# Kernel optimization log

Hardware: AMD Instinct MI355X
Metric: run time of the kernel (lower is better)

The kernel has to match this reference:

```python
import jax, jax.numpy as jnp
import numpy as np

GROUP = 128  # W4A16 quantization group size along the input (reduction) dim


def dequant(q, s, z):
    """Dequantize int4 weights. q: [out, in] ints in [0,16); s, z: [out, in//GROUP]."""
    out_f, in_f = q.shape
    g = in_f // GROUP
    qf = q.reshape(out_f, g, GROUP).astype(s.dtype)
    w = (qf - z[:, :, None]) * s[:, :, None]
    return w.reshape(out_f, in_f)


def setup_inputs() -> dict:
    key = jax.random.key(0)
    ks = jax.random.split(key, 11)
    H, I = 4096, 11008
    B, S = 4, 2048
    x = jax.random.normal(ks[0], (B, S, H), dtype=jnp.float32)
    qw_gate = jax.random.randint(ks[1], (I, H), 0, 16, dtype=jnp.int32)
    qw_up = jax.random.randint(ks[2], (I, H), 0, 16, dtype=jnp.int32)
    qw_down = jax.random.randint(ks[3], (H, I), 0, 16, dtype=jnp.int32)
    # scales small so dequantized weights have realistic magnitude; zeros in [0,16)
    s_gate = jax.random.uniform(ks[4], (I, H // GROUP), dtype=jnp.float32) * 0.01
    z_gate = jax.random.uniform(ks[5], (I, H // GROUP), dtype=jnp.float32) * 16.0
    s_up = jax.random.uniform(ks[6], (I, H // GROUP), dtype=jnp.float32) * 0.01
    z_up = jax.random.uniform(ks[7], (I, H // GROUP), dtype=jnp.float32) * 16.0
    s_down = jax.random.uniform(ks[8], (H, I // GROUP), dtype=jnp.float32) * 0.01
    z_down = jax.random.uniform(ks[9], (H, I // GROUP), dtype=jnp.float32) * 16.0
    return {
        "x": x,
        "qw_gate": qw_gate, "qw_up": qw_up, "qw_down": qw_down,
        "s_gate": s_gate, "z_gate": z_gate,
        "s_up": s_up, "z_up": z_up,
        "s_down": s_down, "z_down": z_down,
    }


def reference(x, qw_gate, qw_up, qw_down, s_gate, z_gate, s_up, z_up, s_down, z_down):
    # W4A16 SwiGLU MLP: down( silu(gate(x)) * up(x) )
    Wg = dequant(qw_gate, s_gate, z_gate)   # [I, H]
    Wu = dequant(qw_up, s_up, z_up)         # [I, H]
    Wd = dequant(qw_down, s_down, z_down)   # [H, I]
    g = jnp.einsum('bsh,ih->bsi', x, Wg)
    u = jnp.einsum('bsh,ih->bsi', x, Wu)
    h = jax.nn.silu(g) * u
    return jnp.einsum('bsi,hi->bsh', h, Wd)
```

## Files before the change

### kernel.cpp

```cpp
#include <hip/hip_runtime.h>
#include <hip/hip_fp16.h>

typedef __attribute__((ext_vector_type(8))) short s16x8;
typedef __attribute__((ext_vector_type(8))) _Float16 f16x8;
typedef __attribute__((ext_vector_type(4))) float f32x4;

__global__ void cvt_f32_to_f16_kernel(const float* __restrict__ in,
                                      __half* __restrict__ out, long n) {
  long i = (long)blockIdx.x * blockDim.x + threadIdx.x;
  long stride = (long)gridDim.x * blockDim.x;
  const float4* p4 = (const float4*)in;
  for (long j = i; j * 8 < n; j += stride) {
    float4 a = p4[j * 2];
    float4 b = p4[j * 2 + 1];
    union { s16x8 v; __half2 h2[4]; } w;
    w.h2[0] = __floats2half2_rn(a.x, a.y);
    w.h2[1] = __floats2half2_rn(a.z, a.w);
    w.h2[2] = __floats2half2_rn(b.x, b.y);
    w.h2[3] = __floats2half2_rn(b.z, b.w);
    *(s16x8*)(out + j * 8) = w.v;
  }
}

__global__ void pack_kernel(const int* __restrict__ q, uint32_t* __restrict__ p,
                            long n8) {
  long i = (long)blockIdx.x * blockDim.x + threadIdx.x;
  long stride = (long)gridDim.x * blockDim.x;
  for (; i < n8; i += stride) {
    int4 a = ((const int4*)q)[2 * i];
    int4 b = ((const int4*)q)[2 * i + 1];
    uint32_t w = (uint32_t)a.x | ((uint32_t)a.y << 4) | ((uint32_t)a.z << 8) |
                 ((uint32_t)a.w << 12) | ((uint32_t)b.x << 16) |
                 ((uint32_t)b.y << 20) | ((uint32_t)b.z << 24) |
                 ((uint32_t)b.w << 28);
    p[i] = w;
  }
}

__device__ __forceinline__ s16x8 dq_compute(int4 q0, int4 q1, float s, float z) {
  __half hs = __float2half(s);
  __half2 s2 = __halves2half2(hs, hs);
  __half hc = __float2half(-(64.f + z) * s);
  __half2 c2 = __halves2half2(hc, hc);
  uint32_t b0 = 0x54005400u + ((uint32_t)q0.x << 4) + ((uint32_t)q0.y << 20);
  uint32_t b1 = 0x54005400u + ((uint32_t)q0.z << 4) + ((uint32_t)q0.w << 20);
  uint32_t b2 = 0x54005400u + ((uint32_t)q1.x << 4) + ((uint32_t)q1.y << 20);
  uint32_t b3 = 0x54005400u + ((uint32_t)q1.z << 4) + ((uint32_t)q1.w << 20);
  union { s16x8 v; __half2 h2[4]; } w;
  w.h2[0] = __hfma2(*(__half2*)&b0, s2, c2);
  w.h2[1] = __hfma2(*(__half2*)&b1, s2, c2);
  w.h2[2] = __hfma2(*(__half2*)&b2, s2, c2);
  w.h2[3] = __hfma2(*(__half2*)&b3, s2, c2);
  return w.v;
}

__device__ __forceinline__ s16x8 dq8(uint32_t w, __half2 s2, __half2 c2) {
  union { s16x8 v; __half2 h2[4]; } r;
#pragma unroll
  for (int i = 0; i < 4; ++i) {
    uint32_t t = (w >> (8 * i)) & 0xFFu;
    uint32_t b = 0x54005400u + ((t & 15u) << 4) + ((t >> 4) << 20);
    r.h2[i] = __hfma2(*(__half2*)&b, s2, c2);
  }
  return r.v;
}

__device__ __forceinline__ int xcd_swz(int w0, int nwg) {
  const int q = nwg >> 3, r = nwg & 7;
  const int xcd = w0 & 7, idx = w0 >> 3;
  const int base = (xcd < r) ? xcd * (q + 1) : r * (q + 1) + (xcd - r) * q;
  return base + idx;
}

template <int PKG, int PKU>
__global__ __launch_bounds__(512, 2)
void gateup_kernel(const __half* __restrict__ Xh,
                   const int* __restrict__ Qg, const uint32_t* __restrict__ Pg,
                   const int* __restrict__ Qu, const uint32_t* __restrict__ Pu,
                   const float* __restrict__ Sg, const float* __restrict__ Zg,
                   const float* __restrict__ Su, const float* __restrict__ Zu,
                   __half* __restrict__ Pan, int mbs) {
  constexpr int H = 4096, I = 11008, G = 32;
  const int wg = xcd_swz(blockIdx.x, gridDim.x);
  const int mb = wg % mbs;
  const int nb = wg / mbs;
  const int m0 = mb * 256;
  const int n0 = nb * 128;
  const int tid = threadIdx.x;
  const int lane = tid & 63;
  const int wave = tid >> 6;
  const int wm = (wave >> 1) * 64, wn = (wave & 1) * 64;
  const int l15 = lane & 15, lq = lane >> 4;
  const int rsw = (l15 & 7) << 3;

  __shared__ __half As[2][256][64];
  __shared__ __half Bg[2][128][64];
  __shared__ __half Bu[2][128][64];

  f32x4 accg[4][4], accu[4][4];
#pragma unroll
  for (int i = 0; i < 4; ++i)
#pragma unroll
    for (int j = 0; j < 4; ++j) {
      accg[i][j] = {0.f, 0.f, 0.f, 0.f};
      accu[i][j] = {0.f, 0.f, 0.f, 0.f};
    }

  const int arowD = tid >> 3;
  const int acolD = (((tid & 7) ^ ((tid >> 3) & 7)) << 3);
  const int qrow = tid >> 2, qcol0 = (tid & 3) * 16, qsw = (qrow & 7) << 3;
  const int*      qPg = Qg + (size_t)(n0 + qrow) * H + qcol0;
  const int*      qPu = Qu + (size_t)(n0 + qrow) * H + qcol0;
  const uint32_t* pPg = Pg + (size_t)(n0 + qrow) * (H / 8) + (tid & 3) * 2;
  const uint32_t* pPu = Pu + (size_t)(n0 + qrow) * (H / 8) + (tid & 3) * 2;
  const float* sPg = Sg + (size_t)(n0 + qrow) * G;
  const float* zPg = Zg + (size_t)(n0 + qrow) * G;
  const float* sPu = Su + (size_t)(n0 + qrow) * G;
  const float* zPu = Zu + (size_t)(n0 + qrow) * G;

  int4 qG[4], qU[4];
  uint32_t wG0, wG1, wU0, wU1;
  float sG, zG, sU, zU;

#define STAGE_A(buf, kk)                                              \
  {                                                                   \
    const int _k = (kk);                                              \
    _Pragma("unroll")                                                 \
    for (int c = 0; c < 4; ++c) {                                     \
      const __half* src = Xh + (size_t)(m0 + c * 64 + arowD) * H + _k + acolD; \
      __half* dst = &As[buf][0][0] + (size_t)(c * 512 + tid) * 8;     \
      __builtin_amdgcn_global_load_lds((const __attribute__((address_space(1))) void*)src, \
                                       (__attribute__((address_space(3))) void*)dst, 16, 0, 0); \
    }                                                                 \
  }
#define LOAD_Q(kk)                                                    \
  {                                                                   \
    const int _k = (kk);                                              \
    if (PKG) { wG0 = pPg[_k >> 3]; wG1 = pPg[(_k >> 3) + 1]; }        \
    else {                                                            \
      _Pragma("unroll")                                               \
      for (int i = 0; i < 4; ++i) qG[i] = ((const int4*)(qPg + _k))[i]; \
    }                                                                 \
    if (PKU) { wU0 = pPu[_k >> 3]; wU1 = pPu[(_k >> 3) + 1]; }        \
    else {                                                            \
      _Pragma("unroll")                                               \
      for (int i = 0; i < 4; ++i) qU[i] = ((const int4*)(qPu + _k))[i]; \
    }                                                                 \
    sG = sPg[_k >> 7]; zG = zPg[_k >> 7];                             \
    sU = sPu[_k >> 7]; zU = zPu[_k >> 7];                             \
  }
#define WRITE_B(buf)                                                  \
  {                                                                   \
    if (PKG) {                                                        \
      __half h1 = __float2half(sG);                                   \
      __half2 s2 = __halves2half2(h1, h1);                            \
      __half h2 = __float2half(-(64.f + zG) * sG);                    \
      __half2 c2 = __halves2half2(h2, h2);                            \
      *(s16x8*)&Bg[buf][qrow][(qcol0 + 0) ^ qsw] = dq8(wG0, s2, c2);  \
      *(s16x8*)&Bg[buf][qrow][(qcol0 + 8) ^ qsw] = dq8(wG1, s2, c2);  \
    } else {                                                          \
      *(s16x8*)&Bg[buf][qrow][(qcol0 + 0) ^ qsw] = dq_compute(qG[0], qG[1], sG, zG); \
      *(s16x8*)&Bg[buf][qrow][(qcol0 + 8) ^ qsw] = dq_compute(qG[2], qG[3], sG, zG); \
    }                                                                 \
    if (PKU) {                                                        \
      __half h3 = __float2half(sU);                                   \
      __half2 s3 = __halves2half2(h3, h3);                            \
      __half h4 = __float2half(-(64.f + zU) * sU);                    \
      __half2 c3 = __halves2half2(h4, h4);                            \
      *(s16x8*)&Bu[buf][qrow][(qcol0 + 0) ^ qsw] = dq8(wU0, s3, c3);  \
      *(s16x8*)&Bu[buf][qrow][(qcol0 + 8) ^ qsw] = dq8(wU1, s3, c3);  \
    } else {                                                          \
      *(s16x8*)&Bu[buf][qrow][(qcol0 + 0) ^ qsw] = dq_compute(qU[0], qU[1], sU, zU); \
      *(s16x8*)&Bu[buf][qrow][(qcol0 + 8) ^ qsw] = dq_compute(qU[2], qU[3], sU, zU); \
    }                                                                 \
  }
#define MFMA_BUF(buf)                                                 \
  {                                                                   \
    __builtin_amdgcn_s_setprio(1);                                    \
    _Pragma("unroll")                                                 \
    for (int kk = 0; kk < 2; ++kk) {                                  \
      const int cbase = (kk * 32 + lq * 8) ^ rsw;                     \
      f16x8 af[4];                                                    \
      _Pragma("unroll")                                               \
      for (int i = 0; i < 4; ++i)                                     \
        af[i] = *(const f16x8*)&As[buf][wm + i * 16 + l15][cbase];    \
      _Pragma("unroll")                                               \
      for (int j = 0; j < 4; ++j) {                                   \
        f16x8 bg = *(const f16x8*)&Bg[buf][wn + j * 16 + l15][cbase]; \
        f16x8 bu = *(const f16x8*)&Bu[buf][wn + j * 16 + l15][cbase]; \
        _Pragma("unroll")                                             \
        for (int i = 0; i < 4; ++i) {                                 \
          accg[i][j] = __builtin_amdgcn_mfma_f32_16x16x32_f16(af[i], bg, accg[i][j], 0, 0, 0); \
          accu[i][j] = __builtin_amdgcn_mfma_f32_16x16x32_f16(af[i], bu, accu[i][j], 0, 0, 0); \
        }                                                             \
      }                                                               \
    }                                                                 \
    __builtin_amdgcn_s_setprio(0);                                    \
  }

  const int nt = H / 64;
  STAGE_A(0, 0)
  LOAD_Q(0)
  WRITE_B(0)
  __syncthreads();

  int p = 0;
  for (int t = 0; t < nt; ++t) {
    if (t + 1 < nt) {
      STAGE_A(p ^ 1, (t + 1) * 64)
      LOAD_Q((t + 1) * 64)
    }
    MFMA_BUF(p)
    if (t + 1 < nt) WRITE_B(p ^ 1)
    __syncthreads();
    p ^= 1;
  }
#undef STAGE_A
#undef LOAD_Q
#undef WRITE_B
#undef MFMA_BUF

#pragma unroll
  for (int i = 0; i < 4; ++i)
#pragma unroll
    for (int j = 0; j < 4; ++j)
#pragma unroll
      for (int r = 0; r < 4; ++r) {
        const int row = m0 + wm + i * 16 + lq * 4 + r;
        const int col = n0 + wn + j * 16 + l15;
        float g = accg[i][j][r];
        float u = accu[i][j][r];
        float hv = (g / (1.f + __expf(-g))) * u;
        Pan[(size_t)row * I + col] = __float2half(hv);
      }
}

template <int PK>
__global__ __launch_bounds__(512, 2)
void down_kernel(const __half* __restrict__ Hws,
                 const int* __restrict__ Qd, const uint32_t* __restrict__ QdP,
                 const float* __restrict__ Sd, const float* __restrict__ Zd,
                 float* __restrict__ Out, int mbs) {
  constexpr int K = 11008, N = 4096, G = 86;
  const int wg = xcd_swz(blockIdx.x, gridDim.x);
  const int mb = wg % mbs;
  const int nb = wg / mbs;
  const int m0 = mb * 256, n0 = nb * 128;
  const int tid = threadIdx.x;
  const int lane = tid & 63;
  const int wave = tid >> 6;
  const int wm = (wave >> 1) * 64, wn = (wave & 1) * 64;
  const int l15 = lane & 15, lq = lane >> 4;
  const int rsw = (l15 & 7) << 3;

  __shared__ __half As[2][256][64];
  __shared__ __half Bs[2][128][64];

  f32x4 acc[4][4];
#pragma unroll
  for (int i = 0; i < 4; ++i)
#pragma unroll
    for (int j = 0; j < 4; ++j) acc[i][j] = {0.f, 0.f, 0.f, 0.f};

  const int arowD = tid >> 3;
  const int acolD = (((tid & 7) ^ ((tid >> 3) & 7)) << 3);
  const int qrow = tid >> 2, qcol0 = (tid & 3) * 16, qsw = (qrow & 7) << 3;
  const int*      qP  = Qd  + (size_t)(n0 + qrow) * K + qcol0;
  const uint32_t* qPp = QdP + (size_t)(n0 + qrow) * (K / 8) + (tid & 3) * 2;
  const float* sP = Sd + (size_t)(n0 + qrow) * G;
  const float* zP = Zd + (size_t)(n0 + qrow) * G;

  int4 qA[4], qB[4];
  uint32_t wA0, wA1, wB0, wB1;
  float sA, zA, sB, zB;

#define STAGE_A(buf, kk)                                              \
  {                                                                   \
    const int _k = (kk);                                              \
    _Pragma("unroll")                                                 \
    for (int c = 0; c < 4; ++c) {                                     \
      const __half* src = Hws + (size_t)(m0 + c * 64 + arowD) * K + _k + acolD; \
      __half* dst = &As[buf][0][0] + (size_t)(c * 512 + tid) * 8;     \
      __builtin_amdgcn_global_load_lds((const __attribute__((address_space(1))) void*)src, \
                                       (__attribute__((address_space(3))) void*)dst, 16, 0, 0); \
    }                                                                 \
  }
#define LOAD_Q(set, kk)                                               \
  {                                                                   \
    const int _k = (kk);                                              \
    if (PK) {                                                         \
      w##set##0 = qPp[_k >> 3]; w##set##1 = qPp[(_k >> 3) + 1];       \
    } else {                                                          \
      _Pragma("unroll")                                               \
      for (int i = 0; i < 4; ++i) q##set[i] = ((const int4*)(qP + _k))[i]; \
    }                                                                 \
    s##set = sP[_k >> 7]; z##set = zP[_k >> 7];                       \
  }
#define WRITE_B(buf, set)                                             \
  {                                                                   \
    if (PK) {                                                         \
      __half hs = __float2half(s##set);                               \
      __half2 s2 = __halves2half2(hs, hs);                            \
      __half hc = __float2half(-(64.f + z##set) * s##set);            \
      __half2 c2 = __halves2half2(hc, hc);                            \
      *(s16x8*)&Bs[buf][qrow][(qcol0 + 0) ^ qsw] = dq8(w##set##0, s2, c2); \
      *(s16x8*)&Bs[buf][qrow][(qcol0 + 8) ^ qsw] = dq8(w##set##1, s2, c2); \
    } else {                                                          \
      *(s16x8*)&Bs[buf][qrow][(qcol0 + 0) ^ qsw] = dq_compute(q##set[0], q##set[1], s##set, z##set); \
      *(s16x8*)&Bs[buf][qrow][(qcol0 + 8) ^ qsw] = dq_compute(q##set[2], q##set[3], s##set, z##set); \
    }                                                                 \
  }
#define MFMA_BUF(buf)                                                 \
  {                                                                   \
    __builtin_amdgcn_s_setprio(1);                                    \
    _Pragma("unroll")                                                 \
    for (int kk = 0; kk < 2; ++kk) {                                  \
      const int cbase = (kk * 32 + lq * 8) ^ rsw;                     \
      f16x8 af[4];                                                    \
      _Pragma("unroll")                                               \
      for (int i = 0; i < 4; ++i)                                     \
        af[i] = *(const f16x8*)&As[buf][wm + i * 16 + l15][cbase];    \
      _Pragma("unroll")                                               \
      for (int j = 0; j < 4; ++j) {                                   \
        f16x8 bf = *(const f16x8*)&Bs[buf][wn + j * 16 + l15][cbase]; \
        _Pragma("unroll")                                             \
        for (int i = 0; i < 4; ++i)                                   \
          acc[i][j] = __builtin_amdgcn_mfma_f32_16x16x32_f16(af[i], bf, acc[i][j], 0, 0, 0); \
      }                                                               \
    }                                                                 \
    __builtin_amdgcn_s_setprio(0);                                    \
  }

  const int nt = K / 64;
  STAGE_A(0, 0)
  LOAD_Q(A, 0)
  LOAD_Q(B, 64)
  WRITE_B(0, A)
  __syncthreads();

  for (int t = 0; t < nt; t += 2) {
    if (t + 1 < nt) STAGE_A(1, (t + 1) * 64)
    if (t + 2 < nt) LOAD_Q(A, (t + 2) * 64)
    MFMA_BUF(0)
    if (t + 1 < nt) WRITE_B(1, B)
    __syncthreads();
    if (t + 2 < nt) STAGE_A(0, (t + 2) * 64)
    if (t + 3 < nt) LOAD_Q(B, (t + 3) * 64)
    MFMA_BUF(1)
    if (t + 2 < nt) WRITE_B(0, A)
    __syncthreads();
  }
#undef STAGE_A
#undef LOAD_Q
#undef WRITE_B
#undef MFMA_BUF

#pragma unroll
  for (int i = 0; i < 4; ++i)
#pragma unroll
    for (int j = 0; j < 4; ++j)
#pragma unroll
      for (int r = 0; r < 4; ++r) {
        const int row = m0 + wm + i * 16 + lq * 4 + r;
        const int col = n0 + wn + j * 16 + l15;
        Out[(size_t)row * N + col] = acc[i][j][r];
      }
}

extern "C" void kernel_launch(void* const* d_in, const int* in_sizes, int n_in,
                              void* d_out, int out_size, void* d_ws, size_t ws_size,
                              hipStream_t stream) {
  const float* x  = (const float*)d_in[0];
  const int* qg   = (const int*)d_in[1];
  const int* qu   = (const int*)d_in[2];
  const int* qd   = (const int*)d_in[3];
  const float* sg = (const float*)d_in[4];
  const float* zg = (const float*)d_in[5];
  const float* su = (const float*)d_in[6];
  const float* zu = (const float*)d_in[7];
  const float* sd = (const float*)d_in[8];
  const float* zd = (const float*)d_in[9];
  float* out = (float*)d_out;

  const int M = 8192, H = 4096, I = 11008;
  const long N8 = (long)I * H / 8;

  const int PD_MAX = 1375, PG_MAX = 2751, PU_MAX = 4127;
  uint32_t* Pd = (uint32_t*)d_out;
  uint32_t* Pg = Pd + N8;
  uint32_t* Pu = Pg + N8;

  pack_kernel<<<2048, 256, 0, stream>>>(qd, Pd, N8);
  pack_kernel<<<2048, 256, 0, stream>>>(qg, Pg, N8);
  pack_kernel<<<2048, 256, 0, stream>>>(qu, Pu, N8);

  long mc = (long)(ws_size / ((size_t)I * 2));
  mc &= ~255L;
  if (mc > 2048) mc = 2048;
  if (mc < 256) mc = 256;
  const int Mc = (int)mc;
  __half* wsh = (__half*)d_ws;

  int mb_arr[64], mbs_arr[64];
  int nch = 0;
  for (int mb = 0; mb < M; mb += Mc) {
    mb_arr[nch] = mb;
    mbs_arr[nch] = ((M - mb < Mc) ? (M - mb) : Mc) / 256;
    ++nch;
  }

  int destr = M;
  for (int c = nch - 1; c >= 0; --c) {
    const int mbase = mb_arr[c];
    const int mbs = mbs_arr[c];
    const int rows = mbs * 256;
    const int xrows = rows / 2;
    const int wsxlo = mbase + rows - xrows;
    __half* wsx = (__half*)(out + (size_t)wsxlo * H);

    cvt_f32_to_f16_kernel<<<1024, 256, 0, stream>>>(
        x + (size_t)mbase * H, wsx, (long)rows * H);
    if (wsxlo < destr) destr = wsxlo;

    const bool g_pk = (PG_MAX < destr);
    const bool u_pk = (PU_MAX < destr);
    const bool d_pk = (PD_MAX < destr) && (PD_MAX < mbase);

    if (g_pk && u_pk)
      gateup_kernel<1, 1><<<mbs * (I / 128), 512, 0, stream>>>(
          wsx, qg, Pg, qu, Pu, sg, zg, su, zu, wsh, mbs);
    else if (g_pk)
      gateup_kernel<1, 0><<<mbs * (I / 128), 512, 0, stream>>>(
          wsx, qg, Pg, qu, Pu, sg, zg, su, zu, wsh, mbs);
    else
      gateup_kernel<0, 0><<<mbs * (I / 128), 512, 0, stream>>>(
          wsx, qg, Pg, qu, Pu, sg, zg, su, zu, wsh, mbs);

    if (d_pk)
      down_kernel<1><<<mbs * 32, 512, 0, stream>>>(
          wsh, qd, Pd, sd, zd, out + (size_t)mbase * H, mbs);
    else
      down_kernel<0><<<mbs * 32, 512, 0, stream>>>(
          wsh, qd, Pd, sd, zd, out + (size_t)mbase * H, mbs);

    if (mbase < destr) destr = mbase;
  }
}
```

Before: 3.039 ms.

## Fuse pack/convert prep and fold next chunk's x conversion into GEMM grids

```diff
diff --git a/kernel.cpp b/kernel.cpp
--- a/kernel.cpp
+++ b/kernel.cpp
@@ -5,35 +5,51 @@
 typedef __attribute__((ext_vector_type(8))) _Float16 f16x8;
 typedef __attribute__((ext_vector_type(4))) float f32x4;
 
+__device__ __forceinline__ void cvt_unit(const float4* __restrict__ p4,
+                                         __half* __restrict__ out, long j) {
+  float4 a = p4[j * 2];
+  float4 b = p4[j * 2 + 1];
+  union { s16x8 v; __half2 h2[4]; } w;
+  w.h2[0] = __floats2half2_rn(a.x, a.y);
+  w.h2[1] = __floats2half2_rn(a.z, a.w);
+  w.h2[2] = __floats2half2_rn(b.x, b.y);
+  w.h2[3] = __floats2half2_rn(b.z, b.w);
+  *(s16x8*)(out + j * 8) = w.v;
+}
+
 __global__ void cvt_f32_to_f16_kernel(const float* __restrict__ in,
-                                      __half* __restrict__ out, long n) {
+                                      __half* __restrict__ out, long n8) {
   long i = (long)blockIdx.x * blockDim.x + threadIdx.x;
   long stride = (long)gridDim.x * blockDim.x;
   const float4* p4 = (const float4*)in;
-  for (long j = i; j * 8 < n; j += stride) {
-    float4 a = p4[j * 2];
-    float4 b = p4[j * 2 + 1];
-    union { s16x8 v; __half2 h2[4]; } w;
-    w.h2[0] = __floats2half2_rn(a.x, a.y);
-    w.h2[1] = __floats2half2_rn(a.z, a.w);
-    w.h2[2] = __floats2half2_rn(b.x, b.y);
-    w.h2[3] = __floats2half2_rn(b.z, b.w);
-    *(s16x8*)(out + j * 8) = w.v;
-  }
-}
-
-__global__ void pack_kernel(const int* __restrict__ q, uint32_t* __restrict__ p,
-                            long n8) {
+  for (long j = i; j < n8; j += stride) cvt_unit(p4, out, j);
+}
+
+__device__ __forceinline__ void pack_unit(const int* __restrict__ q,
+                                          uint32_t* __restrict__ p, long i) {
+  int4 a = ((const int4*)q)[2 * i];
+  int4 b = ((const int4*)q)[2 * i + 1];
+  p[i] = (uint32_t)a.x | ((uint32_t)a.y << 4) | ((uint32_t)a.z << 8) |
+         ((uint32_t)a.w << 12) | ((uint32_t)b.x << 16) |
+         ((uint32_t)b.y << 20) | ((uint32_t)b.z << 24) |
+         ((uint32_t)b.w << 28);
+}
+
+__global__ void prep_kernel(const int* __restrict__ qd, uint32_t* __restrict__ Pd,
+                            const int* __restrict__ qg, uint32_t* __restrict__ Pg,
+                            const int* __restrict__ qu, uint32_t* __restrict__ Pu,
+                            long n8,
+                            const float* __restrict__ xc, __half* __restrict__ wsx,
+                            long ncvt) {
   long i = (long)blockIdx.x * blockDim.x + threadIdx.x;
   long stride = (long)gridDim.x * blockDim.x;
-  for (; i < n8; i += stride) {
-    int4 a = ((const int4*)q)[2 * i];
-    int4 b = ((const int4*)q)[2 * i + 1];
-    uint32_t w = (uint32_t)a.x | ((uint32_t)a.y << 4) | ((uint32_t)a.z << 8) |
-                 ((uint32_t)a.w << 12) | ((uint32_t)b.x << 16) |
-                 ((uint32_t)b.y << 20) | ((uint32_t)b.z << 24) |
-                 ((uint32_t)b.w << 28);
-    p[i] = w;
+  const long total = 3 * n8 + ncvt;
+  const float4* p4 = (const float4*)xc;
+  for (; i < total; i += stride) {
+    if (i < n8) pack_unit(qd, Pd, i);
+    else if (i < 2 * n8) pack_unit(qg, Pg, i - n8);
+    else if (i < 3 * n8) pack_unit(qu, Pu, i - 2 * n8);
+    else cvt_unit(p4, wsx, i - 3 * n8);
   }
 }
 
@@ -79,9 +95,20 @@
                    const int* __restrict__ Qu, const uint32_t* __restrict__ Pu,
                    const float* __restrict__ Sg, const float* __restrict__ Zg,
                    const float* __restrict__ Su, const float* __restrict__ Zu,
-                   __half* __restrict__ Pan, int mbs) {
+                   __half* __restrict__ Pan, int mbs,
+                   const float* __restrict__ xnext, __half* __restrict__ wsxn,
+                   long ncvt) {
   constexpr int H = 4096, I = 11008, G = 32;
   const int wg = xcd_swz(blockIdx.x, gridDim.x);
+  const int gemmBlocks = mbs * (I / 128);
+  if (wg >= gemmBlocks) {
+    const int ncb = gridDim.x - gemmBlocks;
+    long i = (long)(wg - gemmBlocks) * 512 + threadIdx.x;
+    long stride = (long)ncb * 512;
+    const float4* p4 = (const float4*)xnext;
+    for (long j = i; j < ncvt; j += stride) cvt_unit(p4, wsxn, j);
+    return;
+  }
   const int mb = wg % mbs;
   const int nb = wg / mbs;
   const int m0 = mb * 256;
@@ -240,9 +267,20 @@
 void down_kernel(const __half* __restrict__ Hws,
                  const int* __restrict__ Qd, const uint32_t* __restrict__ QdP,
                  const float* __restrict__ Sd, const float* __restrict__ Zd,
-                 float* __restrict__ Out, int mbs) {
+                 float* __restrict__ Out, int mbs,
+                 const float* __restrict__ xnext, __half* __restrict__ wsxn,
+                 long ncvt) {
   constexpr int K = 11008, N = 4096, G = 86;
   const int wg = xcd_swz(blockIdx.x, gridDim.x);
+  const int gemmBlocks = mbs * 32;
+  if (wg >= gemmBlocks) {
+    const int ncb = gridDim.x - gemmBlocks;
+    long i = (long)(wg - gemmBlocks) * 512 + threadIdx.x;
+    long stride = (long)ncb * 512;
+    const float4* p4 = (const float4*)xnext;
+    for (long j = i; j < ncvt; j += stride) cvt_unit(p4, wsxn, j);
+    return;
+  }
   const int mb = wg % mbs;
   const int nb = wg / mbs;
   const int m0 = mb * 256, n0 = nb * 128;
@@ -385,14 +423,11 @@
   const int M = 8192, H = 4096, I = 11008;
   const long N8 = (long)I * H / 8;
 
-  const int PD_MAX = 1375, PG_MAX = 2751, PU_MAX = 4127;
+  const int PD_LO = 0, PD_HI = 1376, PG_LO = 1376, PG_HI = 2752,
+            PU_LO = 2752, PU_HI = 4128;
   uint32_t* Pd = (uint32_t*)d_out;
   uint32_t* Pg = Pd + N8;
   uint32_t* Pu = Pg + N8;
-
-  pack_kernel<<<2048, 256, 0, stream>>>(qd, Pd, N8);
-  pack_kernel<<<2048, 256, 0, stream>>>(qg, Pg, N8);
-  pack_kernel<<<2048, 256, 0, stream>>>(qu, Pu, N8);
 
   long mc = (long)(ws_size / ((size_t)I * 2));
   mc &= ~255L;
@@ -409,40 +444,80 @@
     ++nch;
   }
 
+  auto wsx_lo = [&](int c) {
+    const int rows = mbs_arr[c] * 256;
+    return mb_arr[c] + rows - rows / 2;
+  };
+  auto wsx_ptr = [&](int c) { return (__half*)(out + (size_t)wsx_lo(c) * H); };
+  auto overlap = [](int a0, int a1, int b0, int b1) {
+    return a0 < b1 && b0 < a1;
+  };
+
+  {
+    const int c0 = nch - 1;
+    prep_kernel<<<2048, 256, 0, stream>>>(
+        qd, Pd, qg, Pg, qu, Pu, N8,
+        x + (size_t)mb_arr[c0] * H, wsx_ptr(c0),
+        (long)mbs_arr[c0] * 256 * H / 8);
+  }
+
   int destr = M;
+  if (wsx_lo(nch - 1) < destr) destr = wsx_lo(nch - 1);
+
   for (int c = nch - 1; c >= 0; --c) {
     const int mbase = mb_arr[c];
     const int mbs = mbs_arr[c];
-    const int rows = mbs * 256;
-    const int xrows = rows / 2;
-    const int wsxlo = mbase + rows - xrows;
-    __half* wsx = (__half*)(out + (size_t)wsxlo * H);
-
-    cvt_f32_to_f16_kernel<<<1024, 256, 0, stream>>>(
-        x + (size_t)mbase * H, wsx, (long)rows * H);
-    if (wsxlo < destr) destr = wsxlo;
-
-    const bool g_pk = (PG_MAX < destr);
-    const bool u_pk = (PU_MAX < destr);
-    const bool d_pk = (PD_MAX < destr) && (PD_MAX < mbase);
-
-    if (g_pk && u_pk)
-      gateup_kernel<1, 1><<<mbs * (I / 128), 512, 0, stream>>>(
-          wsx, qg, Pg, qu, Pu, sg, zg, su, zu, wsh, mbs);
-    else if (g_pk)
-      gateup_kernel<1, 0><<<mbs * (I / 128), 512, 0, stream>>>(
-          wsx, qg, Pg, qu, Pu, sg, zg, su, zu, wsh, mbs);
-    else
-      gateup_kernel<0, 0><<<mbs * (I / 128), 512, 0, stream>>>(
-          wsx, qg, Pg, qu, Pu, sg, zg, su, zu, wsh, mbs);
-
-    if (d_pk)
-      down_kernel<1><<<mbs * 32, 512, 0, stream>>>(
-          wsh, qd, Pd, sd, zd, out + (size_t)mbase * H, mbs);
-    else
-      down_kernel<0><<<mbs * 32, 512, 0, stream>>>(
-          wsh, qd, Pd, sd, zd, out + (size_t)mbase * H, mbs);
+    const bool g_pk = (PG_HI <= destr);
+    const bool u_pk = (PU_HI <= destr);
+    const bool d_pk = (PD_HI <= destr) && (PD_HI <= mbase);
+
+    bool foldG = false, foldD = false;
+    long ncvt = 0;
+    const float* xn = x;
+    __half* wsxn = nullptr;
+    if (c > 0) {
+      const int lo = wsx_lo(c - 1);
+      const int hi = mb_arr[c - 1] + mbs_arr[c - 1] * 256;
+      ncvt = (long)mbs_arr[c - 1] * 256 * H / 8;
+      xn = x + (size_t)mb_arr[c - 1] * H;
+      wsxn = wsx_ptr(c - 1);
+      foldG = !((g_pk && overlap(lo, hi, PG_LO, PG_HI)) ||
+                (u_pk && overlap(lo, hi, PU_LO, PU_HI)));
+      foldD = !(d_pk && overlap(lo, hi, PD_LO, PD_HI));
+    }
+
+    {
+      const int gb = mbs * (I / 128);
+      const int grid = foldG ? gb + 80 : gb;
+      const long nc = foldG ? ncvt : 0;
+      if (g_pk && u_pk)
+        gateup_kernel<1, 1><<<grid, 512, 0, stream>>>(
+            wsx_ptr(c), qg, Pg, qu, Pu, sg, zg, su, zu, wsh, mbs, xn, wsxn, nc);
+      else if (g_pk)
+        gateup_kernel<1, 0><<<grid, 512, 0, stream>>>(
+            wsx_ptr(c), qg, Pg, qu, Pu, sg, zg, su, zu, wsh, mbs, xn, wsxn, nc);
+      else
+        gateup_kernel<0, 0><<<grid, 512, 0, stream>>>(
+            wsx_ptr(c), qg, Pg, qu, Pu, sg, zg, su, zu, wsh, mbs, xn, wsxn, nc);
+    }
+
+    {
+      const bool fD = !foldG && foldD && (c > 0);
+      const int gb = mbs * 32;
+      const int grid = fD ? gb + 80 : gb;
+      const long nc = fD ? ncvt : 0;
+      if (d_pk)
+        down_kernel<1><<<grid, 512, 0, stream>>>(
+            wsh, qd, Pd, sd, zd, out + (size_t)mbase * H, mbs, xn, wsxn, nc);
+      else
+        down_kernel<0><<<grid, 512, 0, stream>>>(
+            wsh, qd, Pd, sd, zd, out + (size_t)mbase * H, mbs, xn, wsxn, nc);
+    }
+
+    if (c > 0 && !foldG && !foldD)
+      cvt_f32_to_f16_kernel<<<1024, 256, 0, stream>>>(xn, wsxn, ncvt);
 
     if (mbase < destr) destr = mbase;
-  }
-}
+    if (c > 0 && wsx_lo(c - 1) < destr) destr = wsx_lo(c - 1);
+  }
+}
```

Measured after the change: 3.275 ms. 7.8% more time.

## Add 128x128-tile down-projection kernel with 256 threads and two blocks per CU

Applied to the files above, without the earlier changes.

```diff
diff --git a/kernel.cpp b/kernel.cpp
--- a/kernel.cpp
+++ b/kernel.cpp
@@ -367,6 +367,134 @@
       }
 }
 
+__global__ __launch_bounds__(256, 2)
+void down128_kernel(const __half* __restrict__ Hws,
+                    const uint32_t* __restrict__ QdP,
+                    const float* __restrict__ Sd, const float* __restrict__ Zd,
+                    float* __restrict__ Out, int mbs2) {
+  constexpr int K = 11008, N = 4096, G = 86;
+  const int wg = xcd_swz(blockIdx.x, gridDim.x);
+  const int mb = wg % mbs2;
+  const int nb = wg / mbs2;
+  const int m0 = mb * 128, n0 = nb * 128;
+  const int tid = threadIdx.x;
+  const int lane = tid & 63;
+  const int wave = tid >> 6;
+  const int wm = (wave >> 1) * 64, wn = (wave & 1) * 64;
+  const int l15 = lane & 15, lq = lane >> 4;
+  const int rsw = (l15 & 7) << 3;
+
+  __shared__ __half As[2][128][64];
+  __shared__ __half Bs[2][128][64];
+
+  f32x4 acc[4][4];
+#pragma unroll
+  for (int i = 0; i < 4; ++i)
+#pragma unroll
+    for (int j = 0; j < 4; ++j) acc[i][j] = {0.f, 0.f, 0.f, 0.f};
+
+  const int arowD = tid >> 3;
+  const int acolD = (((tid & 7) ^ ((tid >> 3) & 7)) << 3);
+  const int qr0 = tid >> 2, qcol0 = (tid & 3) * 16;
+
+  uint32_t wA[4], wB[4];
+  float sA[2], zA[2], sB[2], zB[2];
+
+#define STAGE_A(buf, kk)                                              \
+  {                                                                   \
+    const int _k = (kk);                                              \
+    _Pragma("unroll")                                                 \
+    for (int c = 0; c < 4; ++c) {                                     \
+      const __half* src = Hws + (size_t)(m0 + c * 32 + arowD) * K + _k + acolD; \
+      __half* dst = &As[buf][0][0] + (size_t)(c * 256 + tid) * 8;     \
+      __builtin_amdgcn_global_load_lds((const __attribute__((address_space(1))) void*)src, \
+                                       (__attribute__((address_space(3))) void*)dst, 16, 0, 0); \
+    }                                                                 \
+  }
+#define LOAD_Q(set, kk)                                               \
+  {                                                                   \
+    const int _k = (kk);                                              \
+    _Pragma("unroll")                                                 \
+    for (int ps = 0; ps < 2; ++ps) {                                  \
+      const int rg = n0 + ps * 64 + qr0;                              \
+      const uint32_t* pp = QdP + (size_t)rg * (K / 8) + (tid & 3) * 2 + (_k >> 3); \
+      w##set[ps * 2 + 0] = pp[0];                                     \
+      w##set[ps * 2 + 1] = pp[1];                                     \
+      s##set[ps] = Sd[(size_t)rg * G + (_k >> 7)];                    \
+      z##set[ps] = Zd[(size_t)rg * G + (_k >> 7)];                    \
+    }                                                                 \
+  }
+#define WRITE_B(buf, set)                                             \
+  {                                                                   \
+    _Pragma("unroll")                                                 \
+    for (int ps = 0; ps < 2; ++ps) {                                  \
+      const int r = ps * 64 + qr0;                                    \
+      const int sw = (r & 7) << 3;                                    \
+      __half hs = __float2half(s##set[ps]);                           \
+      __half2 s2 = __halves2half2(hs, hs);                            \
+      __half hc = __float2half(-(64.f + z##set[ps]) * s##set[ps]);    \
+      __half2 c2 = __halves2half2(hc, hc);                            \
+      *(s16x8*)&Bs[buf][r][(qcol0 + 0) ^ sw] = dq8(w##set[ps * 2 + 0], s2, c2); \
+      *(s16x8*)&Bs[buf][r][(qcol0 + 8) ^ sw] = dq8(w##set[ps * 2 + 1], s2, c2); \
+    }                                                                 \
+  }
+#define MFMA_BUF(buf)                                                 \
+  {                                                                   \
+    __builtin_amdgcn_s_setprio(1);                                    \
+    _Pragma("unroll")                                                 \
+    for (int kk = 0; kk < 2; ++kk) {                                  \
+      const int cbase = (kk * 32 + lq * 8) ^ rsw;                     \
+      f16x8 af[4];                                                    \
+      _Pragma("unroll")                                               \
+      for (int i = 0; i < 4; ++i)                                     \
+        af[i] = *(const f16x8*)&As[buf][wm + i * 16 + l15][cbase];    \
+      _Pragma("unroll")                                               \
+      for (int j = 0; j < 4; ++j) {                                   \
+        f16x8 bf = *(const f16x8*)&Bs[buf][wn + j * 16 + l15][cbase]; \
+        _Pragma("unroll")                                             \
+        for (int i = 0; i < 4; ++i)                                   \
+          acc[i][j] = __builtin_amdgcn_mfma_f32_16x16x32_f16(af[i], bf, acc[i][j], 0, 0, 0); \
+      }                                                               \
+    }                                                                 \
+    __builtin_amdgcn_s_setprio(0);                                    \
+  }
+
+  const int nt = K / 64;
+  STAGE_A(0, 0)
+  LOAD_Q(A, 0)
+  LOAD_Q(B, 64)
+  WRITE_B(0, A)
+  __syncthreads();
+
+  for (int t = 0; t < nt; t += 2) {
+    if (t + 1 < nt) STAGE_A(1, (t + 1) * 64)
+    if (t + 2 < nt) LOAD_Q(A, (t + 2) * 64)
+    MFMA_BUF(0)
+    if (t + 1 < nt) WRITE_B(1, B)
+    __syncthreads();
+    if (t + 2 < nt) STAGE_A(0, (t + 2) * 64)
+    if (t + 3 < nt) LOAD_Q(B, (t + 3) * 64)
+    MFMA_BUF(1)
+    if (t + 2 < nt) WRITE_B(0, A)
+    __syncthreads();
+  }
+#undef STAGE_A
+#undef LOAD_Q
+#undef WRITE_B
+#undef MFMA_BUF
+
+#pragma unroll
+  for (int i = 0; i < 4; ++i)
+#pragma unroll
+    for (int j = 0; j < 4; ++j)
+#pragma unroll
+      for (int r = 0; r < 4; ++r) {
+        const int row = m0 + wm + i * 16 + lq * 4 + r;
+        const int col = n0 + wn + j * 16 + l15;
+        Out[(size_t)row * N + col] = acc[i][j][r];
+      }
+}
+
 extern "C" void kernel_launch(void* const* d_in, const int* in_sizes, int n_in,
                               void* d_out, int out_size, void* d_ws, size_t ws_size,
                               hipStream_t stream) {
@@ -437,8 +565,8 @@
           wsx, qg, Pg, qu, Pu, sg, zg, su, zu, wsh, mbs);
 
     if (d_pk)
-      down_kernel<1><<<mbs * 32, 512, 0, stream>>>(
-          wsh, qd, Pd, sd, zd, out + (size_t)mbase * H, mbs);
+      down128_kernel<<<(mbs * 2) * 32, 256, 0, stream>>>(
+          wsh, Pd, sd, zd, out + (size_t)mbase * H, mbs * 2);
     else
       down_kernel<0><<<mbs * 32, 512, 0, stream>>>(
           wsh, qd, Pd, sd, zd, out + (size_t)mbase * H, mbs);
```

Measured after the change: 3.114 ms. 1.02x slower.
